# Kernel tuning notes

Hardware: AMD Instinct MI355X
Metric: run time of the kernel (lower is better)

Reference implementation:

```python
import jax, jax.numpy as jnp
import numpy as np

D_MODEL = 1024
N_HEAD = 8      # KV heads
N_QUERY = 4     # query groups per KV head
D_HEAD = D_MODEL // (N_HEAD * N_QUERY)  # 32
KV_DIM = D_HEAD * N_HEAD                # 256
BATCH, SEQ = 4, 1024
BASE = 10000.0


def _rope(x):
    """Interleaved RoPE as in the torch module. theta denominator is always
    d_model/2 = 512 (layer-level), even when applied to the 256-dim key."""
    d = x.shape[-1]
    d2 = d // 2
    dm2 = D_MODEL // 2
    theta = BASE ** (-jnp.arange(dm2, dtype=jnp.float32) / dm2)  # [512]
    pos = jnp.arange(x.shape[-2], dtype=jnp.float32)
    ang = pos[:, None] * theta[None, :d2]  # [S, d2]
    cos, sin = jnp.cos(ang), jnp.sin(ang)
    xe, xo = x[..., ::2], x[..., 1::2]
    out = jnp.stack([xe * cos - xo * sin, xo * cos + xe * sin], axis=-1)
    return out.reshape(x.shape)


def setup_inputs() -> dict:
    key = jax.random.key(0)
    ks = jax.random.split(key, 6)
    x = jax.random.normal(ks[0], (BATCH, SEQ, D_MODEL), dtype=jnp.float32)
    s = 0.02
    Wq = jax.random.normal(ks[1], (D_MODEL, D_MODEL), dtype=jnp.float32) * s
    Wk = jax.random.normal(ks[2], (KV_DIM, D_MODEL), dtype=jnp.float32) * s
    Wv = jax.random.normal(ks[3], (KV_DIM, D_MODEL), dtype=jnp.float32) * s
    Wo = jax.random.normal(ks[4], (D_MODEL, D_MODEL), dtype=jnp.float32) * s
    bo = jnp.zeros((D_MODEL,), dtype=jnp.float32)
    # causal mask: True = masked out
    causal = jnp.triu(jnp.ones((SEQ, SEQ), dtype=bool), k=1)
    mask = jnp.broadcast_to(causal[None, None], (BATCH, 1, SEQ, SEQ))
    return {"x": x, "Wq": Wq, "Wk": Wk, "Wv": Wv, "Wo": Wo, "bo": bo, "mask": mask}


def reference(x, Wq, Wk, Wv, Wo, bo, mask):
    n_b, n_seq, _ = x.shape
    q = _rope(x @ Wq.T)                 # [B,S,1024]
    k = _rope(x @ Wk.T)                 # [B,S,256]
    v = x @ Wv.T                        # [B,S,256]
    # head split; KV heads repeat-interleaved n_query times to match query heads
    qh = q.reshape(n_b, n_seq, N_QUERY * N_HEAD, D_HEAD).transpose(0, 2, 1, 3)
    kh = jnp.repeat(k.reshape(n_b, n_seq, N_HEAD, D_HEAD), N_QUERY, axis=2).transpose(0, 2, 1, 3)
    vh = jnp.repeat(v.reshape(n_b, n_seq, N_HEAD, D_HEAD), N_QUERY, axis=2).transpose(0, 2, 1, 3)
    scale = 1.0 / jnp.sqrt(jnp.float32(D_HEAD))
    scores = jnp.einsum('bhqd,bhkd->bhqk', qh, kh) * scale
    scores = jnp.where(mask, jnp.float32(-1e9), scores)
    probs = jax.nn.softmax(scores, axis=-1)
    probs = jnp.where(mask, jnp.float32(0.0), probs)
    out = jnp.einsum('bhqk,bhkd->bqhd', probs, vh)  # [B,S,32,32]
    out = out.reshape(n_b, n_seq, D_MODEL)
    return out @ Wo.T + bo
```

## Files before the change

### kernel.cpp

```cpp
#include <hip/hip_runtime.h>
#include <hip/hip_bf16.h>

typedef __attribute__((ext_vector_type(8))) short short8;
typedef __attribute__((ext_vector_type(4))) short short4v;
typedef __attribute__((ext_vector_type(4))) float float4v;

#define DEV __device__ __forceinline__

constexpr int SEQ = 1024;
constexpr int DM  = 1024;
constexpr int KVD = 256;
constexpr int MTOK = 4096;

constexpr float QSCALE = 0.25503487660444f;


DEV void load_lds16(const void* g, void* l) {
  __builtin_amdgcn_global_load_lds(
      (const __attribute__((address_space(1))) unsigned int*)g,
      (__attribute__((address_space(3))) unsigned int*)l, 16, 0, 0);
}

DEV unsigned short f2bf(float f) {
  unsigned int u = __float_as_uint(f);
  u += 0x7fffu + ((u >> 16) & 1u);
  return (unsigned short)(u >> 16);
}

DEV float fexp2(float x) {
  float y;
  asm("v_exp_f32 %0, %1" : "=v"(y) : "v"(x));
  return y;
}

DEV unsigned int cvtpk(float lo, float hi) {
  unsigned int r;
  asm("v_cvt_pk_bf16_f32 %0, %1, %2" : "=v"(r) : "v"(lo), "v"(hi));
  return r;
}

#if __has_builtin(__builtin_amdgcn_mfma_f32_16x16x16bf16_1k)
DEV float4v mfma16(short4v a, short4v b, float4v c) {
  return __builtin_amdgcn_mfma_f32_16x16x16bf16_1k(a, b, c, 0, 0, 0);
}
#else
DEV float4v mfma16(short4v a, short4v b, float4v c) {
  asm("v_mfma_f32_16x16x16_bf16 %0, %1, %2, %0" : "+v"(c) : "v"(a), "v"(b));
  return c;
}
#endif

#define WAIT_VM(N)  asm volatile("s_waitcnt vmcnt(" #N ")" ::: "memory")
#define WAIT_LG(N)  asm volatile("s_waitcnt lgkmcnt(" #N ")" ::: "memory")
#define WAIT_LGKM0  asm volatile("s_waitcnt lgkmcnt(0)" ::: "memory")
#define SBAR0       __builtin_amdgcn_sched_barrier(0)


__global__ __launch_bounds__(256)
void prep_kernel(const float* __restrict__ x,  const float* __restrict__ Wq,
                 const float* __restrict__ Wk, const float* __restrict__ Wv,
                 const float* __restrict__ Wo,
                 unsigned short* __restrict__ xb, unsigned short* __restrict__ Wqkvb,
                 unsigned short* __restrict__ Wob,
                 float* __restrict__ rc, float* __restrict__ rs)
{
  const int NX  = (MTOK*DM)/4;
  const int NWQ = (DM*DM)/4;
  const int NWK = (KVD*DM)/4;
  const int NCONV = NX + NWQ + 2*NWK + NWQ;
  int id = blockIdx.x*256 + threadIdx.x;
  if (id < NCONV) {
    const float* src; unsigned short* dst; int u;
    if      (id < NX)            { src = x;  dst = xb;                     u = id; }
    else if (id < NX+NWQ)        { src = Wq; dst = Wqkvb;                  u = id-NX; }
    else if (id < NX+NWQ+NWK)    { src = Wk; dst = Wqkvb + DM*DM;          u = id-(NX+NWQ); }
    else if (id < NX+NWQ+2*NWK)  { src = Wv; dst = Wqkvb + DM*DM+KVD*DM;   u = id-(NX+NWQ+NWK); }
    else                         { src = Wo; dst = Wob;                    u = id-(NX+NWQ+2*NWK); }
    float4 v = ((const float4*)src)[u];
    ushort4 o;
    o.x = f2bf(v.x); o.y = f2bf(v.y); o.z = f2bf(v.z); o.w = f2bf(v.w);
    ((ushort4*)dst)[u] = o;
  } else {
    int id2 = id - NCONV;
    if (id2 < SEQ*512) {
      int pos = id2 >> 9, i = id2 & 511;
      float theta = exp2f((float)i * (-13.287712379549449f/512.0f));
      float ang = (float)pos * theta;
      float sv, cv; sincosf(ang, &sv, &cv);
      rc[id2] = cv; rs[id2] = sv;
    }
  }
}


template<int MODE, int GY>
__global__ __launch_bounds__(256)
void gemm_nt(const unsigned short* __restrict__ A, const unsigned short* __restrict__ Bw,
             unsigned short* __restrict__ outQ, unsigned short* __restrict__ outK,
             unsigned short* __restrict__ outVt, float* __restrict__ outF,
             const float* __restrict__ bias,
             const float* __restrict__ rc, const float* __restrict__ rs)
{
  __shared__ __align__(16) unsigned short As[2][128*64];
  __shared__ __align__(16) unsigned short Bs[2][64*64];
  const int tid = threadIdx.x;
  const int w  = tid >> 6, l = tid & 63;
  const int lg = l >> 4, ll = l & 15;
  const int wr = w >> 1, wc = w & 1;

  const int bid = (int)blockIdx.x;
  const int f   = (bid & 7) * (4*GY) + (bid >> 3);
  const int brow = (f / GY) * 128, bcol = (f % GY) * 64;

  float4v acc[4][2];
#pragma unroll
  for (int i = 0; i < 4; ++i)
#pragma unroll
    for (int j = 0; j < 2; ++j) acc[i][j] = (float4v){0.f,0.f,0.f,0.f};

  auto stage = [&](int kt, int cur) {
#pragma unroll
    for (int blk = 0; blk < 4; ++blk) {
      int cid = blk*256 + w*64 + l;
      int row = cid >> 3, c = cid & 7;
      int cg = c ^ (row & 7);
      load_lds16(A + (size_t)(brow+row)*DM + kt*64 + cg*8,
                 &As[cur][(blk*256 + w*64)*8]);
    }
#pragma unroll
    for (int blk = 0; blk < 2; ++blk) {
      int cid = blk*256 + w*64 + l;
      int row = cid >> 3, c = cid & 7;
      int cg = c ^ (row & 7);
      load_lds16(Bw + (size_t)(bcol+row)*DM + kt*64 + cg*8,
                 &Bs[cur][(blk*256 + w*64)*8]);
    }
  };

  stage(0, 0); stage(1, 1);
#pragma unroll 1
  for (int kt = 0; kt < 16; ++kt) {
    const int cur = kt & 1;
    if (kt < 15) { WAIT_VM(6); }
    else         { WAIT_VM(0); }
    __builtin_amdgcn_s_barrier();

    short8 af[2][4], bf[2][2];
#pragma unroll
    for (int mi = 0; mi < 4; ++mi) {
      int row = wr*64 + mi*16 + ll;
      af[0][mi] = *(const short8*)&As[cur][row*64 + ((lg ^ (row & 7)) << 3)];
    }
#pragma unroll
    for (int ni = 0; ni < 2; ++ni) {
      int col = wc*32 + ni*16 + ll;
      bf[0][ni] = *(const short8*)&Bs[cur][col*64 + ((lg ^ (col & 7)) << 3)];
    }
    SBAR0;
#pragma unroll
    for (int mi = 0; mi < 4; ++mi) {
      int row = wr*64 + mi*16 + ll;
      af[1][mi] = *(const short8*)&As[cur][row*64 + (((4 + lg) ^ (row & 7)) << 3)];
    }
#pragma unroll
    for (int ni = 0; ni < 2; ++ni) {
      int col = wc*32 + ni*16 + ll;
      bf[1][ni] = *(const short8*)&Bs[cur][col*64 + (((4 + lg) ^ (col & 7)) << 3)];
    }
    WAIT_LG(6);
    SBAR0;
    __builtin_amdgcn_s_setprio(1);
#pragma unroll
    for (int mi = 0; mi < 4; ++mi)
#pragma unroll
      for (int ni = 0; ni < 2; ++ni)
        acc[mi][ni] = __builtin_amdgcn_mfma_f32_16x16x32_bf16(af[0][mi], bf[0][ni], acc[mi][ni], 0,0,0);
    __builtin_amdgcn_s_setprio(0);
    SBAR0;
    WAIT_LGKM0;
    SBAR0;
    __builtin_amdgcn_s_barrier();

    if (kt + 2 < 16) stage(kt + 2, cur);

    __builtin_amdgcn_s_setprio(1);
#pragma unroll
    for (int mi = 0; mi < 4; ++mi)
#pragma unroll
      for (int ni = 0; ni < 2; ++ni)
        acc[mi][ni] = __builtin_amdgcn_mfma_f32_16x16x32_bf16(af[1][mi], bf[1][ni], acc[mi][ni], 0,0,0);
    __builtin_amdgcn_s_setprio(0);
  }

#pragma unroll
  for (int mi = 0; mi < 4; ++mi)
#pragma unroll
    for (int ni = 0; ni < 2; ++ni)
#pragma unroll
      for (int r = 0; r < 4; ++r) {
        int m = brow + wr*64 + mi*16 + lg*4 + r;
        int n = bcol + wc*32 + ni*16 + ll;
        float v = acc[mi][ni][r];
        if constexpr (MODE == 0) {
          float p = __shfl_xor(v, 1);
          if (n < DM) {
            int pos = m & (SEQ-1);
            int i = n >> 1;
            float ct = rc[pos*512 + i], st = rs[pos*512 + i];
            v = (n & 1) ? (v*ct + p*st) : (v*ct - p*st);
            outQ[(size_t)m*DM + n] = f2bf(v * QSCALE);
          } else if (n < DM + KVD) {
            int nk = n - DM;
            int pos = m & (SEQ-1);
            int i = nk >> 1;
            float ct = rc[pos*512 + i], st = rs[pos*512 + i];
            v = (nk & 1) ? (v*ct + p*st) : (v*ct - p*st);
            outK[(size_t)m*KVD + nk] = f2bf(v);
          } else {
            int nv = n - DM - KVD;
            outVt[((size_t)(m >> 10)*KVD + nv)*SEQ + (m & (SEQ-1))] = f2bf(v);
          }
        } else {
          outF[(size_t)m*DM + n] = v + bias[n];
        }
      }
}


__global__ __launch_bounds__(256)
void attn_kernel(const unsigned short* __restrict__ Qb, const unsigned short* __restrict__ Kb,
                 const unsigned short* __restrict__ Vtb, unsigned short* __restrict__ Ob)
{
  __shared__ __align__(16) unsigned short Kl[3][64*32];
  __shared__ __align__(16) unsigned short Vl[3][32*64];
  const int tid = threadIdx.x;
  const int w  = tid >> 6, l = tid & 63;
  const int lg = l >> 4, ll = l & 15;
  const int hk = blockIdx.y, b = blockIdx.z;
  const int h  = hk*4 + w;

  auto stage = [&](int kvt, int bi) {
    int kv = tid >> 2, c = tid & 3, cl = c ^ ((kv >> 1) & 3);
    load_lds16(&Kb[((size_t)b*SEQ + kvt*64 + kv)*KVD + hk*32 + cl*8],
               &Kl[bi][(w*64)*8]);
    int d = tid >> 3, c8 = tid & 7, cl8 = c8 ^ (d & 7);
    load_lds16(&Vtb[((size_t)b*KVD + hk*32 + d)*SEQ + kvt*64 + cl8*8],
               &Vl[bi][(w*64)*8]);
  };

#pragma unroll 1
  for (int ph = 0; ph < 2; ++ph) {
    const int qt = ph ? (int)blockIdx.x : 31 - (int)blockIdx.x;
    const int nt = qt/2 + 1;
    const int q0 = qt*32;

    short8 qf[2];
#pragma unroll
    for (int qi = 0; qi < 2; ++qi)
      qf[qi] = *(const short8*)&Qb[((size_t)b*SEQ + q0 + qi*16 + ll)*DM + h*32 + (lg<<3)];

    float4v o[2][2];
    float mrow[2] = {-1e30f, -1e30f};
    float lrow[2] = {0.f, 0.f};
#pragma unroll
    for (int qi = 0; qi < 2; ++qi)
#pragma unroll
      for (int df = 0; df < 2; ++df) o[qi][df] = (float4v){0,0,0,0};

    WAIT_VM(0);
    stage(0, 0);
    if (1 < nt) stage(1, 1);
    if (2 < nt) stage(2, 2);

    int bi = 0;
    for (int kvt = 0; kvt < nt; ++kvt) {
      if (kvt + 3 <= nt)      { WAIT_VM(4); }
      else if (kvt + 2 == nt) { WAIT_VM(2); }
      else                    { WAIT_VM(0); }
      __builtin_amdgcn_s_barrier();

      short8 kf[4];
#pragma unroll
      for (int ni = 0; ni < 4; ++ni) {
        int kv = ni*16 + ll;
        kf[ni] = *(const short8*)&Kl[bi][kv*32 + ((lg ^ ((kv>>1)&3)) << 3)];
      }
      short4v vf[2][4];
#pragma unroll
      for (int df = 0; df < 2; ++df) {
        int d = df*16 + ll;
#pragma unroll
        for (int ni = 0; ni < 4; ++ni) {
          int ch = ((ni*2 + (lg>>1)) ^ (d & 7));
          vf[df][ni] = *(const short4v*)&Vl[bi][d*64 + (ch<<3) + ((lg&1)<<2)];
        }
      }
      WAIT_LGKM0;
      __builtin_amdgcn_sched_barrier(0);
      __builtin_amdgcn_s_barrier();

      if (kvt + 3 < nt) stage(kvt + 3, bi);

      float sc[2][4][4];
      __builtin_amdgcn_s_setprio(1);
#pragma unroll
      for (int qi = 0; qi < 2; ++qi)
#pragma unroll
        for (int ni = 0; ni < 4; ++ni) {
          float4v s = __builtin_amdgcn_mfma_f32_16x16x32_bf16(kf[ni], qf[qi],
                         (float4v){0,0,0,0}, 0,0,0);
#pragma unroll
          for (int r = 0; r < 4; ++r) sc[qi][ni][r] = s[r];
        }
      __builtin_amdgcn_s_setprio(0);

      if (kvt == nt-1) {
#pragma unroll
        for (int qi = 0; qi < 2; ++qi) {
          int q = q0 + qi*16 + ll;
#pragma unroll
          for (int ni = 0; ni < 4; ++ni)
#pragma unroll
            for (int r = 0; r < 4; ++r) {
              int kv = kvt*64 + ni*16 + lg*4 + r;
              if (kv > q) sc[qi][ni][r] = -1e30f;
            }
        }
      }

      short4v pf[2][4];
#pragma unroll
      for (int qi = 0; qi < 2; ++qi) {
        float mt = fmaxf(fmaxf(fmaxf(sc[qi][0][0], sc[qi][0][1]), fmaxf(sc[qi][0][2], sc[qi][0][3])),
                   fmaxf(fmaxf(sc[qi][1][0], sc[qi][1][1]), fmaxf(sc[qi][1][2], sc[qi][1][3])));
        mt = fmaxf(mt,
             fmaxf(fmaxf(fmaxf(sc[qi][2][0], sc[qi][2][1]), fmaxf(sc[qi][2][2], sc[qi][2][3])),
                   fmaxf(fmaxf(sc[qi][3][0], sc[qi][3][1]), fmaxf(sc[qi][3][2], sc[qi][3][3]))));
        mt = fmaxf(mt, __shfl_xor(mt, 16));
        mt = fmaxf(mt, __shfl_xor(mt, 32));

        const bool grow = !__all(mt <= mrow[qi]);
        float mn = grow ? fmaxf(mrow[qi], mt) : mrow[qi];
        float s0 = 0.f;
#pragma unroll
        for (int ni = 0; ni < 4; ++ni) {
          float p0 = fexp2(sc[qi][ni][0] - mn);
          float p1 = fexp2(sc[qi][ni][1] - mn);
          float p2 = fexp2(sc[qi][ni][2] - mn);
          float p3 = fexp2(sc[qi][ni][3] - mn);
          s0 += (p0 + p1) + (p2 + p3);
          unsigned int w0 = cvtpk(p0, p1), w1 = cvtpk(p2, p3);
          union { unsigned int u[2]; short4v s4; } cv;
          cv.u[0] = w0; cv.u[1] = w1;
          pf[qi][ni] = cv.s4;
        }
        if (grow) {
          float corr = fexp2(mrow[qi] - mn);
          mrow[qi] = mn;
          lrow[qi] = lrow[qi]*corr + s0;
#pragma unroll
          for (int df = 0; df < 2; ++df)
#pragma unroll
            for (int r = 0; r < 4; ++r) o[qi][df][r] *= corr;
        } else {
          lrow[qi] += s0;
        }
      }

      __builtin_amdgcn_s_setprio(1);
#pragma unroll
      for (int qi = 0; qi < 2; ++qi)
#pragma unroll
        for (int df = 0; df < 2; ++df)
#pragma unroll
          for (int ni = 0; ni < 4; ++ni)
            o[qi][df] = mfma16(vf[df][ni], pf[qi][ni], o[qi][df]);
      __builtin_amdgcn_s_setprio(0);

      bi = (bi == 2) ? 0 : bi + 1;
    }

#pragma unroll
    for (int qi = 0; qi < 2; ++qi) {
      float s = lrow[qi];
      s += __shfl_xor(s, 16);
      s += __shfl_xor(s, 32);
      float inv = 1.f / s;
      size_t tok = (size_t)b*SEQ + q0 + qi*16 + ll;
#pragma unroll
      for (int df = 0; df < 2; ++df) {
        short4v sv;
#pragma unroll
        for (int r = 0; r < 4; ++r) sv[r] = (short)f2bf(o[qi][df][r] * inv);
        *(short4v*)&Ob[tok*DM + h*32 + df*16 + lg*4] = sv;
      }
    }
  }
}


extern "C" void kernel_launch(void* const* d_in, const int* in_sizes, int n_in,
                              void* d_out, int out_size, void* d_ws, size_t ws_size,
                              hipStream_t stream)
{
  const float* x  = (const float*)d_in[0];
  const float* Wq = (const float*)d_in[1];
  const float* Wk = (const float*)d_in[2];
  const float* Wv = (const float*)d_in[3];
  const float* Wo = (const float*)d_in[4];
  const float* bo = (const float*)d_in[5];
  float* out = (float*)d_out;

  char* ws = (char*)d_ws;
  const size_t MB = 1u << 20;
  unsigned short* xb    = (unsigned short*)(ws + 0*MB);
  unsigned short* Wqkvb = (unsigned short*)(ws + 8*MB);
  unsigned short* Wob   = (unsigned short*)(ws + 11*MB);
  float*          rc    = (float*)(ws + 13*MB);
  float*          rs    = (float*)(ws + 15*MB);
  unsigned short* Qb    = (unsigned short*)(ws + 17*MB);
  unsigned short* Kb    = (unsigned short*)(ws + 25*MB);
  unsigned short* Vt    = (unsigned short*)(ws + 27*MB);
  unsigned short* Ob    = (unsigned short*)(ws + 29*MB);
  if (ws_size < 37*MB) return;

  {
    const int total = 1703936 + SEQ*512;
    const int blocks = (total + 255) / 256;
    prep_kernel<<<blocks, 256, 0, stream>>>(x, Wq, Wk, Wv, Wo, xb, Wqkvb, Wob, rc, rs);
  }
  gemm_nt<0, 24><<<dim3(768), 256, 0, stream>>>(xb, Wqkvb, Qb, Kb, Vt, nullptr, nullptr, rc, rs);
  attn_kernel<<<dim3(16, 8, 4), 256, 0, stream>>>(Qb, Kb, Vt, Ob);
  gemm_nt<2, 16><<<dim3(512), 256, 0, stream>>>(Ob, Wob, nullptr, nullptr, nullptr, out, bo, rc, rs);
}
```

Measured before the change: 89.32 us.

## Load K/V fragments directly from global into registers with double buffering

Replaces the LDS triple-buffered staging of K and V tiles, done with global_load_lds plus barriers, with direct per-wave global loads into register fragments. Two register sets are ping-ponged so the next tile's loads are issued while the current tile is computed. Q fragments for both phases are also hoisted to kernel start. This removes the LDS traffic and block barriers, at the cost of redundant global/L2 reads, since all four waves of a block load the same K/V, plus less coalesced access and higher register pressure.

```diff
diff --git a/kernel.cpp b/kernel.cpp
--- a/kernel.cpp
+++ b/kernel.cpp
@@ -231,33 +231,30 @@
 void attn_kernel(const unsigned short* __restrict__ Qb, const unsigned short* __restrict__ Kb,
                  const unsigned short* __restrict__ Vtb, unsigned short* __restrict__ Ob)
 {
-  __shared__ __align__(16) unsigned short Kl[3][64*32];
-  __shared__ __align__(16) unsigned short Vl[3][32*64];
   const int tid = threadIdx.x;
   const int w  = tid >> 6, l = tid & 63;
   const int lg = l >> 4, ll = l & 15;
   const int hk = blockIdx.y, b = blockIdx.z;
   const int h  = hk*4 + w;
 
-  auto stage = [&](int kvt, int bi) {
-    int kv = tid >> 2, c = tid & 3, cl = c ^ ((kv >> 1) & 3);
-    load_lds16(&Kb[((size_t)b*SEQ + kvt*64 + kv)*KVD + hk*32 + cl*8],
-               &Kl[bi][(w*64)*8]);
-    int d = tid >> 3, c8 = tid & 7, cl8 = c8 ^ (d & 7);
-    load_lds16(&Vtb[((size_t)b*KVD + hk*32 + d)*SEQ + kvt*64 + cl8*8],
-               &Vl[bi][(w*64)*8]);
-  };
+  const int qtA = 31 - (int)blockIdx.x;
+  const int qtB = (int)blockIdx.x;
+  short8 qfA[2], qfB[2];
+#pragma unroll
+  for (int qi = 0; qi < 2; ++qi) {
+    qfA[qi] = *(const short8*)&Qb[((size_t)b*SEQ + qtA*32 + qi*16 + ll)*DM + h*32 + (lg<<3)];
+    qfB[qi] = *(const short8*)&Qb[((size_t)b*SEQ + qtB*32 + qi*16 + ll)*DM + h*32 + (lg<<3)];
+  }
+
+  const unsigned short* Kh = Kb  + (size_t)b*SEQ*KVD + hk*32 + (lg<<3);
+  const unsigned short* Vh = Vtb + ((size_t)b*KVD + hk*32)*SEQ + (lg<<2);
 
 #pragma unroll 1
   for (int ph = 0; ph < 2; ++ph) {
-    const int qt = ph ? (int)blockIdx.x : 31 - (int)blockIdx.x;
+    const int qt = ph ? qtB : qtA;
     const int nt = qt/2 + 1;
     const int q0 = qt*32;
-
-    short8 qf[2];
-#pragma unroll
-    for (int qi = 0; qi < 2; ++qi)
-      qf[qi] = *(const short8*)&Qb[((size_t)b*SEQ + q0 + qi*16 + ll)*DM + h*32 + (lg<<3)];
+    const short8* qf = ph ? qfB : qfA;
 
     float4v o[2][2];
     float mrow[2] = {-1e30f, -1e30f};
@@ -267,40 +264,20 @@
 #pragma unroll
       for (int df = 0; df < 2; ++df) o[qi][df] = (float4v){0,0,0,0};
 
-    WAIT_VM(0);
-    stage(0, 0);
-    if (1 < nt) stage(1, 1);
-    if (2 < nt) stage(2, 2);
-
-    int bi = 0;
-    for (int kvt = 0; kvt < nt; ++kvt) {
-      if (kvt + 3 <= nt)      { WAIT_VM(4); }
-      else if (kvt + 2 == nt) { WAIT_VM(2); }
-      else                    { WAIT_VM(0); }
-      __builtin_amdgcn_s_barrier();
-
-      short8 kf[4];
-#pragma unroll
-      for (int ni = 0; ni < 4; ++ni) {
-        int kv = ni*16 + ll;
-        kf[ni] = *(const short8*)&Kl[bi][kv*32 + ((lg ^ ((kv>>1)&3)) << 3)];
-      }
-      short4v vf[2][4];
-#pragma unroll
-      for (int df = 0; df < 2; ++df) {
-        int d = df*16 + ll;
-#pragma unroll
-        for (int ni = 0; ni < 4; ++ni) {
-          int ch = ((ni*2 + (lg>>1)) ^ (d & 7));
-          vf[df][ni] = *(const short4v*)&Vl[bi][d*64 + (ch<<3) + ((lg&1)<<2)];
-        }
-      }
-      WAIT_LGKM0;
-      __builtin_amdgcn_sched_barrier(0);
-      __builtin_amdgcn_s_barrier();
-
-      if (kvt + 3 < nt) stage(kvt + 3, bi);
-
+    auto ldK = [&](short8 (&kf)[4], int kvt) {
+#pragma unroll
+      for (int ni = 0; ni < 4; ++ni)
+        kf[ni] = *(const short8*)&Kh[((size_t)kvt*64 + ni*16 + ll)*KVD];
+    };
+    auto ldV = [&](short4v (&vf)[2][4], int kvt) {
+#pragma unroll
+      for (int df = 0; df < 2; ++df)
+#pragma unroll
+        for (int ni = 0; ni < 4; ++ni)
+          vf[df][ni] = *(const short4v*)&Vh[(size_t)(df*16 + ll)*SEQ + kvt*64 + ni*16];
+    };
+
+    auto compute = [&](const short8 (&kf)[4], const short4v (&vf)[2][4], int kvt) {
       float sc[2][4][4];
       __builtin_amdgcn_s_setprio(1);
 #pragma unroll
@@ -376,8 +353,19 @@
           for (int ni = 0; ni < 4; ++ni)
             o[qi][df] = mfma16(vf[df][ni], pf[qi][ni], o[qi][df]);
       __builtin_amdgcn_s_setprio(0);
-
-      bi = (bi == 2) ? 0 : bi + 1;
+    };
+
+    short8 kfA[4], kfB[4];
+    short4v vfA[2][4], vfB[2][4];
+    ldK(kfA, 0); ldV(vfA, 0);
+    int kvt = 0;
+    while (true) {
+      if (kvt + 1 < nt) { ldK(kfB, kvt+1); ldV(vfB, kvt+1); }
+      compute(kfA, vfA, kvt);
+      ++kvt; if (kvt >= nt) break;
+      if (kvt + 1 < nt) { ldK(kfA, kvt+1); ldV(vfA, kvt+1); }
+      compute(kfB, vfB, kvt);
+      ++kvt; if (kvt >= nt) break;
     }
 
 #pragma unroll
```

New measurement: 105.6 us. 18.2% more time.

## Double KV tile to 128 keys per iteration in attention kernel

Applied to the files above, without the earlier changes.

The attention inner loop now processes 128 keys per tile instead of 64. The LDS staging buffers, staging loads, wait counts and swizzles are enlarged to match. The softmax and PV MFMA work is restructured per query fragment to limit register pressure. The aim is to halve loop iterations and barriers per query tile. In exchange it wastes more masked work on the diagonal tile, doubles LDS use (which may reduce occupancy) and raises register use.

```diff
diff --git a/kernel.cpp b/kernel.cpp
--- a/kernel.cpp
+++ b/kernel.cpp
@@ -231,8 +231,8 @@
 void attn_kernel(const unsigned short* __restrict__ Qb, const unsigned short* __restrict__ Kb,
                  const unsigned short* __restrict__ Vtb, unsigned short* __restrict__ Ob)
 {
-  __shared__ __align__(16) unsigned short Kl[3][64*32];
-  __shared__ __align__(16) unsigned short Vl[3][32*64];
+  __shared__ __align__(16) unsigned short Kl[3][128*32];
+  __shared__ __align__(16) unsigned short Vl[3][32*128];
   const int tid = threadIdx.x;
   const int w  = tid >> 6, l = tid & 63;
   const int lg = l >> 4, ll = l & 15;
@@ -240,18 +240,27 @@
   const int h  = hk*4 + w;
 
   auto stage = [&](int kvt, int bi) {
-    int kv = tid >> 2, c = tid & 3, cl = c ^ ((kv >> 1) & 3);
-    load_lds16(&Kb[((size_t)b*SEQ + kvt*64 + kv)*KVD + hk*32 + cl*8],
-               &Kl[bi][(w*64)*8]);
-    int d = tid >> 3, c8 = tid & 7, cl8 = c8 ^ (d & 7);
-    load_lds16(&Vtb[((size_t)b*KVD + hk*32 + d)*SEQ + kvt*64 + cl8*8],
-               &Vl[bi][(w*64)*8]);
+    const int kv0 = kvt*128;
+#pragma unroll
+    for (int blk = 0; blk < 2; ++blk) {
+      int cid = blk*256 + tid;
+      int row = cid >> 2, c = cid & 3, cl = c ^ ((row >> 1) & 3);
+      load_lds16(&Kb[((size_t)b*SEQ + kv0 + row)*KVD + hk*32 + cl*8],
+                 &Kl[bi][(blk*256 + w*64)*8]);
+    }
+#pragma unroll
+    for (int blk = 0; blk < 2; ++blk) {
+      int cid = blk*256 + tid;
+      int d = cid >> 4, c = cid & 15, cl = c ^ (d & 7);
+      load_lds16(&Vtb[((size_t)b*KVD + hk*32 + d)*SEQ + kv0 + cl*8],
+                 &Vl[bi][(blk*256 + w*64)*8]);
+    }
   };
 
 #pragma unroll 1
   for (int ph = 0; ph < 2; ++ph) {
     const int qt = ph ? (int)blockIdx.x : 31 - (int)blockIdx.x;
-    const int nt = qt/2 + 1;
+    const int nt = (qt + 4) >> 2;
     const int q0 = qt*32;
 
     short8 qf[2];
@@ -274,25 +283,25 @@
 
     int bi = 0;
     for (int kvt = 0; kvt < nt; ++kvt) {
-      if (kvt + 3 <= nt)      { WAIT_VM(4); }
-      else if (kvt + 2 == nt) { WAIT_VM(2); }
+      if (kvt + 3 <= nt)      { WAIT_VM(8); }
+      else if (kvt + 2 == nt) { WAIT_VM(4); }
       else                    { WAIT_VM(0); }
       __builtin_amdgcn_s_barrier();
 
-      short8 kf[4];
-#pragma unroll
-      for (int ni = 0; ni < 4; ++ni) {
+      short8 kf[8];
+#pragma unroll
+      for (int ni = 0; ni < 8; ++ni) {
         int kv = ni*16 + ll;
-        kf[ni] = *(const short8*)&Kl[bi][kv*32 + ((lg ^ ((kv>>1)&3)) << 3)];
+        kf[ni] = *(const short8*)&Kl[bi][kv*32 + ((lg ^ ((ll >> 1) & 3)) << 3)];
       }
-      short4v vf[2][4];
+      short4v vf[2][8];
 #pragma unroll
       for (int df = 0; df < 2; ++df) {
         int d = df*16 + ll;
 #pragma unroll
-        for (int ni = 0; ni < 4; ++ni) {
-          int ch = ((ni*2 + (lg>>1)) ^ (d & 7));
-          vf[df][ni] = *(const short4v*)&Vl[bi][d*64 + (ch<<3) + ((lg&1)<<2)];
+        for (int ni = 0; ni < 8; ++ni) {
+          int ch = (ni*2 + (lg >> 1)) ^ (ll & 7);
+          vf[df][ni] = *(const short4v*)&Vl[bi][d*128 + (ch << 3) + ((lg & 1) << 2)];
         }
       }
       WAIT_LGKM0;
@@ -301,58 +310,53 @@
 
       if (kvt + 3 < nt) stage(kvt + 3, bi);
 
-      float sc[2][4][4];
-      __builtin_amdgcn_s_setprio(1);
-#pragma unroll
-      for (int qi = 0; qi < 2; ++qi)
-#pragma unroll
-        for (int ni = 0; ni < 4; ++ni) {
+      const bool lastTile = (kvt == nt-1);
+#pragma unroll
+      for (int qi = 0; qi < 2; ++qi) {
+        float sc[8][4];
+        __builtin_amdgcn_s_setprio(1);
+#pragma unroll
+        for (int ni = 0; ni < 8; ++ni) {
           float4v s = __builtin_amdgcn_mfma_f32_16x16x32_bf16(kf[ni], qf[qi],
                          (float4v){0,0,0,0}, 0,0,0);
 #pragma unroll
-          for (int r = 0; r < 4; ++r) sc[qi][ni][r] = s[r];
-        }
-      __builtin_amdgcn_s_setprio(0);
-
-      if (kvt == nt-1) {
-#pragma unroll
-        for (int qi = 0; qi < 2; ++qi) {
+          for (int r = 0; r < 4; ++r) sc[ni][r] = s[r];
+        }
+        __builtin_amdgcn_s_setprio(0);
+
+        if (lastTile) {
           int q = q0 + qi*16 + ll;
 #pragma unroll
-          for (int ni = 0; ni < 4; ++ni)
+          for (int ni = 0; ni < 8; ++ni)
 #pragma unroll
             for (int r = 0; r < 4; ++r) {
-              int kv = kvt*64 + ni*16 + lg*4 + r;
-              if (kv > q) sc[qi][ni][r] = -1e30f;
+              int kv = kvt*128 + ni*16 + lg*4 + r;
+              if (kv > q) sc[ni][r] = -1e30f;
             }
         }
-      }
-
-      short4v pf[2][4];
-#pragma unroll
-      for (int qi = 0; qi < 2; ++qi) {
-        float mt = fmaxf(fmaxf(fmaxf(sc[qi][0][0], sc[qi][0][1]), fmaxf(sc[qi][0][2], sc[qi][0][3])),
-                   fmaxf(fmaxf(sc[qi][1][0], sc[qi][1][1]), fmaxf(sc[qi][1][2], sc[qi][1][3])));
-        mt = fmaxf(mt,
-             fmaxf(fmaxf(fmaxf(sc[qi][2][0], sc[qi][2][1]), fmaxf(sc[qi][2][2], sc[qi][2][3])),
-                   fmaxf(fmaxf(sc[qi][3][0], sc[qi][3][1]), fmaxf(sc[qi][3][2], sc[qi][3][3]))));
+
+        float mt = fmaxf(fmaxf(sc[0][0], sc[0][1]), fmaxf(sc[0][2], sc[0][3]));
+#pragma unroll
+        for (int ni = 1; ni < 8; ++ni)
+          mt = fmaxf(mt, fmaxf(fmaxf(sc[ni][0], sc[ni][1]), fmaxf(sc[ni][2], sc[ni][3])));
         mt = fmaxf(mt, __shfl_xor(mt, 16));
         mt = fmaxf(mt, __shfl_xor(mt, 32));
 
         const bool grow = !__all(mt <= mrow[qi]);
         float mn = grow ? fmaxf(mrow[qi], mt) : mrow[qi];
         float s0 = 0.f;
-#pragma unroll
-        for (int ni = 0; ni < 4; ++ni) {
-          float p0 = fexp2(sc[qi][ni][0] - mn);
-          float p1 = fexp2(sc[qi][ni][1] - mn);
-          float p2 = fexp2(sc[qi][ni][2] - mn);
-          float p3 = fexp2(sc[qi][ni][3] - mn);
+        short4v pf[8];
+#pragma unroll
+        for (int ni = 0; ni < 8; ++ni) {
+          float p0 = fexp2(sc[ni][0] - mn);
+          float p1 = fexp2(sc[ni][1] - mn);
+          float p2 = fexp2(sc[ni][2] - mn);
+          float p3 = fexp2(sc[ni][3] - mn);
           s0 += (p0 + p1) + (p2 + p3);
           unsigned int w0 = cvtpk(p0, p1), w1 = cvtpk(p2, p3);
           union { unsigned int u[2]; short4v s4; } cv;
           cv.u[0] = w0; cv.u[1] = w1;
-          pf[qi][ni] = cv.s4;
+          pf[ni] = cv.s4;
         }
         if (grow) {
           float corr = fexp2(mrow[qi] - mn);
@@ -365,17 +369,15 @@
         } else {
           lrow[qi] += s0;
         }
+
+        __builtin_amdgcn_s_setprio(1);
+#pragma unroll
+        for (int df = 0; df < 2; ++df)
+#pragma unroll
+          for (int ni = 0; ni < 8; ++ni)
+            o[qi][df] = mfma16(vf[df][ni], pf[ni], o[qi][df]);
+        __builtin_amdgcn_s_setprio(0);
       }
-
-      __builtin_amdgcn_s_setprio(1);
-#pragma unroll
-      for (int qi = 0; qi < 2; ++qi)
-#pragma unroll
-        for (int df = 0; df < 2; ++df)
-#pragma unroll
-          for (int ni = 0; ni < 4; ++ni)
-            o[qi][df] = mfma16(vf[df][ni], pf[qi][ni], o[qi][df]);
-      __builtin_amdgcn_s_setprio(0);
 
       bi = (bi == 2) ? 0 : bi + 1;
     }
```

Result: no change. 90.23 us (+1.0%).
